# Kernel tuning notes

Hardware: AMD Instinct MI355X
Metric: run time of the kernel (lower is better)

Reference implementation:

```python
import jax, jax.numpy as jnp
import numpy as np

# irreps config (l<=1 only)
N, E = 20000, 400000
NS, NV = 64, 32          # node: 64x0e + 32x1o  (dim 64 + 96 = 160)
ES, EV = 8, 8            # edge: 8x0e + 8x1o    (dim 8 + 24 = 32)
HS, HV = 96, 32          # hidden: 96x0e + 32x1o (last HV scalars are gates)
GS = HS - HV             # post-gate scalar channels
INV_SQRT3 = float(1.0 / np.sqrt(3.0))  # w3j(1,1,0) normalization


def _tp_gate(xs, xv, ys, yv, Wss, Wvv, Wsv, Wvs):
    """FullyConnectedTensorProduct (paths 0x0->0, 1.1->0, 0x1->1, 1x0->1)
    with fan-in path normalization, followed by a gated nonlinearity:
    silu on scalars, sigmoid-gated vectors.
    xs:[*,u] xv:[*,u',3] ys:[*,v] yv:[*,v',3] -> (gs:[*,GS], gv:[*,HV,3])"""
    n_s = 1.0 / np.sqrt(Wss.shape[0] * Wss.shape[1] + Wvv.shape[0] * Wvv.shape[1])
    n_v = 1.0 / np.sqrt(Wsv.shape[0] * Wsv.shape[1] + Wvs.shape[0] * Wvs.shape[1])
    hs = (jnp.einsum('eu,ev,uvw->ew', xs, ys, Wss)
          + INV_SQRT3 * jnp.einsum('euk,evk,uvw->ew', xv, yv, Wvv)) * n_s
    hv = (jnp.einsum('eu,evk,uvw->ewk', xs, yv, Wsv)
          + jnp.einsum('euk,ev,uvw->ewk', xv, ys, Wvs)) * n_v
    gs = jax.nn.silu(hs[:, :GS])
    gates = jax.nn.sigmoid(hs[:, GS:])          # [*, HV]
    gv = hv * gates[:, :, None]
    return gs, gv


def _irrep_linear(s, v, Ws, Wv):
    """e3nn-style Linear: independent multiplicity mixing per irrep, 1/sqrt(fan_in)."""
    return (s @ Ws) / np.sqrt(Ws.shape[0]), jnp.einsum('nuk,uw->nwk', v, Wv) / np.sqrt(Wv.shape[0])


def setup_inputs() -> dict:
    key = jax.random.key(0)
    ks = jax.random.split(key, 16)
    inp = {
        'node_features': jax.random.normal(ks[0], (N, NS + 3 * NV), jnp.float32),
        'edge_attr_tensor': jax.random.normal(ks[1], (E, ES + 3 * EV), jnp.float32),
        'node_attr_scalar_raw': jax.random.normal(ks[2], (N, 1), jnp.float32),
        'edge_index': jax.random.randint(ks[3], (2, E), 0, N),
        # message TP weights: node (x) edge -> hidden
        'W_m_ss': jax.random.normal(ks[4], (NS, ES, HS), jnp.float32),
        'W_m_vv': jax.random.normal(ks[5], (NV, EV, HS), jnp.float32),
        'W_m_sv': jax.random.normal(ks[6], (NS, EV, HV), jnp.float32),
        'W_m_vs': jax.random.normal(ks[7], (NV, ES, HV), jnp.float32),
        # linear_messages_out: gate-out (GSx0e+HVx1o) -> hidden
        'Wl_ms': jax.random.normal(ks[8], (GS, HS), jnp.float32),
        'Wl_mv': jax.random.normal(ks[9], (HV, HV), jnp.float32),
        # update TP weights: node (x) hidden -> hidden
        'W_u_ss': jax.random.normal(ks[10], (NS, HS, HS), jnp.float32),
        'W_u_vv': jax.random.normal(ks[11], (NV, HV, HS), jnp.float32),
        'W_u_sv': jax.random.normal(ks[12], (NS, HV, HV), jnp.float32),
        'W_u_vs': jax.random.normal(ks[13], (NV, HS, HV), jnp.float32),
        # linear_update_out: gate-out -> node irreps
        'Wl_us': jax.random.normal(ks[14], (GS, NS), jnp.float32),
        'Wl_uv': jax.random.normal(ks[15], (HV, NV), jnp.float32),
    }
    return inp


def reference(node_features, edge_attr_tensor, node_attr_scalar_raw, edge_index,
              W_m_ss, W_m_vv, W_m_sv, W_m_vs, Wl_ms, Wl_mv,
              W_u_ss, W_u_vv, W_u_sv, W_u_vs, Wl_us, Wl_uv):
    n = node_features.shape[0]
    row, col = edge_index[0], edge_index[1]
    xs = node_features[:, :NS]                              # [N,NS]
    xv = node_features[:, NS:].reshape(n, NV, 3)            # [N,NV,3]
    es = edge_attr_tensor[:, :ES]                           # [E,ES]
    ev = edge_attr_tensor[:, ES:].reshape(-1, EV, 3)        # [E,EV,3]
    # gather source nodes, TP with edge attrs, gate
    ms, mv = _tp_gate(xs[col], xv[col], es, ev, W_m_ss, W_m_vv, W_m_sv, W_m_vs)
    ms, mv = _irrep_linear(ms, mv, Wl_ms, Wl_mv)            # -> hidden irreps
    # scatter-sum into destination nodes
    ags = jax.ops.segment_sum(ms, row, num_segments=n)      # [N,HS]
    agv = jax.ops.segment_sum(mv.reshape(-1, HV * 3), row, num_segments=n).reshape(n, HV, 3)
    # update TP: node (x) aggregated, gate, project back to node irreps
    us, uv = _tp_gate(xs, xv, ags, agv, W_u_ss, W_u_vv, W_u_sv, W_u_vs)
    us, uv = _irrep_linear(us, uv, Wl_us, Wl_uv)
    upd = jnp.concatenate([us, uv.reshape(n, NV * 3)], axis=-1)
    return node_features + upd
```

## Files before the change

kernel.cpp:

```cpp
#include <hip/hip_runtime.h>

#define NN 20000
#define NE 400000

typedef __attribute__((ext_vector_type(4))) float f32x4;
typedef _Float16 h2 __attribute__((ext_vector_type(2)));
typedef _Float16 h8 __attribute__((ext_vector_type(8)));

union H8 { h8 v; h2 p[4]; };

__device__ __forceinline__ float sigf(float x) { return 1.0f / (1.0f + __expf(-x)); }

__device__ __forceinline__ h8 rank1(_Float16 x, const h2 e[4]) {
    h2 xb = {x, x}; H8 f;
    #pragma unroll
    for (int j = 0; j < 4; ++j) f.p[j] = xb * e[j];
    return f.v;
}
__device__ __forceinline__ h8 rank3(_Float16 x0, _Float16 x1, _Float16 x2,
                                    const h2 e0[4], const h2 e1[4], const h2 e2[4]) {
    h2 x0b = {x0, x0}, x1b = {x1, x1}, x2b = {x2, x2}; H8 f;
    #pragma unroll
    for (int j = 0; j < 4; ++j) f.p[j] = x0b * e0[j] + x1b * e1[j] + x2b * e2[j];
    return f.v;
}
#define MFMA(a, b, c) __builtin_amdgcn_mfma_f32_16x16x32_f16(a, b, c, 0, 0, 0)

__global__ __launch_bounds__(256)
void prep_kernel(const float* __restrict__ s1, const float* __restrict__ s2,
                 int K1, int Kt, int Nw, float sc1, float sc2,
                 unsigned short* __restrict__ dst)
{
    __shared__ _Float16 tile[32][34];
    const int tx = threadIdx.x & 31, ty = threadIdx.x >> 5;
    const int K0 = blockIdx.x * 32, w0 = blockIdx.y * 32;
    #pragma unroll
    for (int r = 0; r < 4; ++r) {
        int K = K0 + ty + r * 8, w = w0 + tx;
        if (K < Kt && w < Nw) {
            float v = (K < K1) ? s1[(size_t)K * Nw + w] * sc1
                               : s2[(size_t)(K - K1) * Nw + w] * sc2;
            tile[ty + r * 8][tx] = (_Float16)v;
        }
    }
    __syncthreads();
    #pragma unroll
    for (int r = 0; r < 4; ++r) {
        int w = w0 + ty + r * 8, K = K0 + tx;
        if (w < Nw && K < Kt)
            dst[(size_t)w * Kt + K] = __builtin_bit_cast(unsigned short, tile[tx][ty + r * 8]);
    }
}

__global__ void hist_kernel(const int* __restrict__ eidx, int* __restrict__ counts)
{
    int e = blockIdx.x * 256 + threadIdx.x;
    if (e < NE) atomicAdd(&counts[eidx[e]], 1);
}

__global__ __launch_bounds__(1024)
void scan_kernel(int* __restrict__ data)
{
    __shared__ int wsum[16];
    __shared__ int s_carry;
    const int t = threadIdx.x, lane = t & 63, wv = t >> 6;
    if (t == 0) s_carry = 0;
    __syncthreads();
    for (int base = 0; base < NN; base += 1024) {
        int carry = s_carry;
        int idx = base + t;
        int v = (idx < NN) ? data[idx] : 0;
        int s = v;
        #pragma unroll
        for (int d = 1; d < 64; d <<= 1) {
            int x = __shfl_up(s, d, 64);
            if (lane >= d) s += x;
        }
        if (lane == 63) wsum[wv] = s;
        __syncthreads();
        if (t < 16) {
            int ws = wsum[t];
            #pragma unroll
            for (int d = 1; d < 16; d <<= 1) {
                int x = __shfl_up(ws, d, 64);
                if (t >= d) ws += x;
            }
            wsum[t] = ws;
        }
        __syncthreads();
        if (idx < NN) data[idx] = carry + (wv ? wsum[wv - 1] : 0) + s - v;
        if (t == 0) s_carry = carry + wsum[15];
        __syncthreads();
    }
}

__global__ void scatter_kernel(const int* __restrict__ eidx, int* __restrict__ cursor,
                               int* __restrict__ perm)
{
    int e = blockIdx.x * 256 + threadIdx.x;
    if (e < NE) {
        int r = eidx[e];
        int p = atomicAdd(&cursor[r], 1);
        perm[p] = e;
    }
}

template<int MB>
__device__ __forceinline__ void msg_gemmB(
    int ln, int okt,
    const _Float16 (*s_xsh)[68], const _Float16 (*s_xv01)[66], const _Float16 (*s_xv2)[34],
    const _Float16 (*s_esh)[8], const _Float16 (*s_evTh)[3][8],
    const unsigned short* __restrict__ wB, f32x4* acc)
{
    const unsigned short* b0p = wB + (size_t)ln * 768;
    const unsigned short* b1p = wB + (size_t)(16 + ln) * 768;

    h2 vv[6][4];
    #pragma unroll
    for (int m = 0; m < 6; ++m) {
        const int k = (MB + m) >> 2, e = (((MB + m) & 3) << 4) + ln;
        #pragma unroll
        for (int j = 0; j < 4; ++j) vv[m][j] = ((const h2*)s_evTh[e][k])[j];
    }
    #pragma unroll 4
    for (int ks = 0; ks < 16; ++ks) {
        const int ko = ks * 32 + okt * 8, u = ks * 4 + okt;
        h8 b0 = *(const h8*)(b0p + ko), b1 = *(const h8*)(b1p + ko);
        #pragma unroll
        for (int m = 0; m < 6; ++m) {
            const int e = (((MB + m) & 3) << 4) + ln;
            h8 a = rank1(s_xsh[e][u], vv[m]);
            acc[m * 2]     = MFMA(a, b0, acc[m * 2]);
            acc[m * 2 + 1] = MFMA(a, b1, acc[m * 2 + 1]);
        }
    }
    h2 ee[6][4];
    #pragma unroll
    for (int m = 0; m < 6; ++m) {
        const int e = (((MB + m) & 3) << 4) + ln;
        #pragma unroll
        for (int j = 0; j < 4; ++j) ee[m][j] = ((const h2*)s_esh[e])[j];
    }
    #pragma unroll 4
    for (int ks = 0; ks < 8; ++ks) {
        const int ko = 512 + ks * 32 + okt * 8, u = ks * 4 + okt;
        h8 b0 = *(const h8*)(b0p + ko), b1 = *(const h8*)(b1p + ko);
        #pragma unroll
        for (int m = 0; m < 6; ++m) {
            const int k = (MB + m) >> 2, e = (((MB + m) & 3) << 4) + ln;
            _Float16 x = (k < 2) ? s_xv01[e][u * 2 + k] : s_xv2[e][u];
            h8 a = rank1(x, ee[m]);
            acc[m * 2]     = MFMA(a, b0, acc[m * 2]);
            acc[m * 2 + 1] = MFMA(a, b1, acc[m * 2 + 1]);
        }
    }
}

__global__ __launch_bounds__(256, 3)
void msg_kernel(const float* __restrict__ nf, const float* __restrict__ ea,
                const int* __restrict__ eidx, const int* __restrict__ perm,
                const unsigned short* __restrict__ wA,
                const unsigned short* __restrict__ wB,
                float* __restrict__ agg)
{
    const int e0 = blockIdx.x * 64;
    const int t = threadIdx.x;
    const int wid = t >> 6, lane = t & 63, ln = lane & 15, okt = lane >> 4;

    __shared__ __align__(16) char smem[25600];
    _Float16 (*s_xsh)[68]    = (_Float16(*)[68])(smem);
    _Float16 (*s_xv01)[66]   = (_Float16(*)[66])(smem + 8704);
    _Float16 (*s_xv2)[34]    = (_Float16(*)[34])(smem + 17152);
    _Float16 (*s_esh)[8]     = (_Float16(*)[8])(smem + 21504);
    _Float16 (*s_evTh)[3][8] = (_Float16(*)[3][8])(smem + 22528);
    _Float16 (*s_msg)[162]   = (_Float16(*)[162])(smem);
    _Float16 (*s_gate)[33]   = (_Float16(*)[33])(smem + 20736);

    __shared__ int s_row[64], s_col[64], s_pe[64];

    if (t < 64) {
        int p = perm[e0 + t];
        s_pe[t] = p;
        s_row[t] = eidx[p];
        s_col[t] = eidx[NE + p];
    }
    __syncthreads();
    for (int i = t; i < 64 * 32; i += 256) {
        int e = i >> 5, c = i & 31;
        float v = ea[(size_t)s_pe[e] * 32 + c];
        if (c < 8) s_esh[e][c] = (_Float16)v;
        else { int d = c - 8; s_evTh[e][d % 3][d / 3] = (_Float16)v; }
    }
    for (int i = t; i < 64 * 40; i += 256) {
        int e = i / 40, q = i - e * 40;
        f32x4 f4 = *((const f32x4*)nf + (size_t)s_col[e] * 40 + q);
        if (q < 16) {
            #pragma unroll
            for (int j = 0; j < 4; ++j) s_xsh[e][q * 4 + j] = (_Float16)f4[j];
        } else {
            #pragma unroll
            for (int j = 0; j < 4; ++j) {
                int d = (q - 16) * 4 + j, u = d / 3, k = d - u * 3;
                if (k < 2) s_xv01[e][u * 2 + k] = (_Float16)f4[j];
                else       s_xv2[e][u] = (_Float16)f4[j];
            }
        }
    }
    __syncthreads();

    f32x4 acc[12] = {};

    if (wid < 2) {
        const unsigned short* wb = wA + (size_t)(wid * 48 + ln) * 768;
        h2 esv[4][4];
        #pragma unroll
        for (int m = 0; m < 4; ++m)
            #pragma unroll
            for (int j = 0; j < 4; ++j) esv[m][j] = ((const h2*)s_esh[m * 16 + ln])[j];
        #pragma unroll 4
        for (int ks = 0; ks < 16; ++ks) {
            const int ko = ks * 32 + okt * 8, u = ks * 4 + okt;
            h8 b0 = *(const h8*)(wb + ko);
            h8 b1 = *(const h8*)(wb + 16 * 768 + ko);
            h8 b2 = *(const h8*)(wb + 32 * 768 + ko);
            #pragma unroll
            for (int m = 0; m < 4; ++m) {
                h8 a = rank1(s_xsh[m * 16 + ln][u], esv[m]);
                acc[m * 3 + 0] = MFMA(a, b0, acc[m * 3 + 0]);
                acc[m * 3 + 1] = MFMA(a, b1, acc[m * 3 + 1]);
                acc[m * 3 + 2] = MFMA(a, b2, acc[m * 3 + 2]);
            }
        }
        h2 ev0[4][4], ev1[4][4], ev2[4][4];
        #pragma unroll
        for (int m = 0; m < 4; ++m)
            #pragma unroll
            for (int j = 0; j < 4; ++j) {
                ev0[m][j] = ((const h2*)s_evTh[m * 16 + ln][0])[j];
                ev1[m][j] = ((const h2*)s_evTh[m * 16 + ln][1])[j];
                ev2[m][j] = ((const h2*)s_evTh[m * 16 + ln][2])[j];
            }
        #pragma unroll 4
        for (int ks = 0; ks < 8; ++ks) {
            const int ko = 512 + ks * 32 + okt * 8, u = ks * 4 + okt;
            h8 b0 = *(const h8*)(wb + ko);
            h8 b1 = *(const h8*)(wb + 16 * 768 + ko);
            h8 b2 = *(const h8*)(wb + 32 * 768 + ko);
            #pragma unroll
            for (int m = 0; m < 4; ++m) {
                h2 x01 = *(const h2*)&s_xv01[m * 16 + ln][u * 2];
                h8 a = rank3(x01[0], x01[1], s_xv2[m * 16 + ln][u], ev0[m], ev1[m], ev2[m]);
                acc[m * 3 + 0] = MFMA(a, b0, acc[m * 3 + 0]);
                acc[m * 3 + 1] = MFMA(a, b1, acc[m * 3 + 1]);
                acc[m * 3 + 2] = MFMA(a, b2, acc[m * 3 + 2]);
            }
        }
    } else if (wid == 2) {
        msg_gemmB<0>(ln, okt, s_xsh, s_xv01, s_xv2, s_esh, s_evTh, wB, acc);
    } else {
        msg_gemmB<6>(ln, okt, s_xsh, s_xv01, s_xv2, s_esh, s_evTh, wB, acc);
    }

    __syncthreads();

    if (wid < 2) {
        #pragma unroll
        for (int m = 0; m < 4; ++m)
            #pragma unroll
            for (int j = 0; j < 3; ++j)
                #pragma unroll
                for (int r = 0; r < 4; ++r) {
                    int e = m * 16 + okt * 4 + r;
                    int w = wid * 48 + j * 16 + ln;
                    float h = acc[m * 3 + j][r];
                    if (w < 64) s_msg[e][w] = (_Float16)(h * sigf(h));
                    else        s_gate[e][w - 64] = (_Float16)sigf(h);
                }
    }
    __syncthreads();
    if (wid >= 2) {
        const int mb = (wid - 2) * 6;
        #pragma unroll
        for (int m = 0; m < 6; ++m) {
            int mm = mb + m, k = mm >> 2;
            #pragma unroll
            for (int tt = 0; tt < 2; ++tt)
                #pragma unroll
                for (int r = 0; r < 4; ++r) {
                    int e = ((mm & 3) << 4) + okt * 4 + r;
                    int w2 = tt * 16 + ln;
                    s_msg[e][64 + w2 * 3 + k] =
                        (_Float16)(acc[m * 2 + tt][r] * (float)s_gate[e][w2]);
                }
        }
    }
    __syncthreads();

    if (t < 160) {
        int cur = s_row[0];
        float a = (float)s_msg[0][t];
        for (int e = 1; e < 64; ++e) {
            int r = s_row[e];
            float v = (float)s_msg[e][t];
            if (r != cur) {
                atomicAdd(agg + (size_t)cur * 160 + t, a);
                cur = r; a = v;
            } else a += v;
        }
        atomicAdd(agg + (size_t)cur * 160 + t, a);
    }
}

template<int KH>
__global__ __launch_bounds__(256, 4)
void upd1_kernel(const float* __restrict__ nf, const float* __restrict__ agg,
                 const unsigned short* __restrict__ wA,
                 const unsigned short* __restrict__ wB,
                 const float* __restrict__ Wlms, const float* __restrict__ Wlmv,
                 float* __restrict__ hpart)
{
    const int n0 = blockIdx.x * 32;
    const int t = threadIdx.x;
    const int wid = t >> 6, lane = t & 63, ln = lane & 15, okt = lane >> 4;

    __shared__ __align__(16) _Float16 s_xsh[32][68];
    __shared__ __align__(16) _Float16 s_xv01[32][66];
    __shared__ __align__(16) _Float16 s_xv2[32][34];
    __shared__ __align__(16) _Float16 s_ash[32][104];
    __shared__ __align__(16) _Float16 s_avTh[32][3][40];

    for (int i = t; i < 32 * 40; i += 256) {
        int n = i / 40, q = i - n * 40;
        f32x4 f4 = *((const f32x4*)nf + (size_t)(n0 + n) * 40 + q);
        if (q < 16) {
            #pragma unroll
            for (int j = 0; j < 4; ++j) s_xsh[n][q * 4 + j] = (_Float16)f4[j];
        } else {
            #pragma unroll
            for (int j = 0; j < 4; ++j) {
                int d = (q - 16) * 4 + j, u = d / 3, k = d - u * 3;
                if (k < 2) s_xv01[n][u * 2 + k] = (_Float16)f4[j];
                else       s_xv2[n][u] = (_Float16)f4[j];
            }
        }
    }
    const float* agr = agg + (size_t)n0 * 160;
    #pragma unroll
    for (int r = 0; r < 12; ++r) {
        int o = t + r * 256;
        int n = o / 96, q = o - n * 96;
        float a = 0.f;
        #pragma unroll
        for (int u = 0; u < 64; ++u) a = fmaf(agr[n * 160 + u], Wlms[u * 96 + q], a);
        s_ash[n][q] = (_Float16)(a * 0.125f);
    }
    #pragma unroll
    for (int r = 0; r < 12; ++r) {
        int o = t + r * 256;
        int n = o / 96, q = o - n * 96, k = q >> 5, v = q & 31;
        float a = 0.f;
        #pragma unroll
        for (int u = 0; u < 32; ++u) a = fmaf(agr[n * 160 + 64 + u * 3 + k], Wlmv[u * 32 + v], a);
        s_avTh[n][k][v] = (_Float16)(a * 0.17677669529663687f);
    }
    __syncthreads();

    f32x4 acc[6] = {};
    constexpr int KB0 = KH ? 37 : 0;
    constexpr int KB1 = KH ? 64 : 37;

    if (wid < 2) {
        const unsigned short* wb = wA + (size_t)(wid * 48 + ln) * 7168;
        #pragma unroll 2
        for (int kb = KB0; kb < KB1; ++kb) {
            _Float16 x0 = s_xsh[ln][kb];
            _Float16 x1 = s_xsh[16 + ln][kb];
            #pragma unroll
            for (int p = 0; p < 3; ++p) {
                const int ko = kb * 96 + p * 32 + okt * 8;
                const int v0 = p * 32 + okt * 8;
                h8 b0 = *(const h8*)(wb + ko);
                h8 b1 = *(const h8*)(wb + 16 * 7168 + ko);
                h8 b2 = *(const h8*)(wb + 32 * 7168 + ko);
                h8 a0 = rank1(x0, (const h2*)&s_ash[ln][v0]);
                h8 a1 = rank1(x1, (const h2*)&s_ash[16 + ln][v0]);
                acc[0] = MFMA(a0, b0, acc[0]); acc[1] = MFMA(a0, b1, acc[1]); acc[2] = MFMA(a0, b2, acc[2]);
                acc[3] = MFMA(a1, b0, acc[3]); acc[4] = MFMA(a1, b1, acc[4]); acc[5] = MFMA(a1, b2, acc[5]);
            }
        }
        if (KH) {
            #pragma unroll 4
            for (int ks = 0; ks < 32; ++ks) {
                const int ko = 6144 + ks * 32 + okt * 8;
                const int v0 = okt * 8;
                h8 b0 = *(const h8*)(wb + ko);
                h8 b1 = *(const h8*)(wb + 16 * 7168 + ko);
                h8 b2 = *(const h8*)(wb + 32 * 7168 + ko);
                h2 xa = *(const h2*)&s_xv01[ln][ks * 2];
                h2 xb = *(const h2*)&s_xv01[16 + ln][ks * 2];
                h8 a0 = rank3(xa[0], xa[1], s_xv2[ln][ks],
                              (const h2*)&s_avTh[ln][0][v0], (const h2*)&s_avTh[ln][1][v0],
                              (const h2*)&s_avTh[ln][2][v0]);
                h8 a1 = rank3(xb[0], xb[1], s_xv2[16 + ln][ks],
                              (const h2*)&s_avTh[16 + ln][0][v0], (const h2*)&s_avTh[16 + ln][1][v0],
                              (const h2*)&s_avTh[16 + ln][2][v0]);
                acc[0] = MFMA(a0, b0, acc[0]); acc[1] = MFMA(a0, b1, acc[1]); acc[2] = MFMA(a0, b2, acc[2]);
                acc[3] = MFMA(a1, b0, acc[3]); acc[4] = MFMA(a1, b1, acc[4]); acc[5] = MFMA(a1, b2, acc[5]);
            }
        }
    } else {
        const unsigned short* bp = wB + (size_t)((wid - 2) * 16 + ln) * 5120;
        if (!KH) {
            #pragma unroll 2
            for (int ks = 0; ks < 64; ++ks) {
                const int ko = ks * 32 + okt * 8;
                const int v0 = okt * 8;
                h8 b = *(const h8*)(bp + ko);
                #pragma unroll
                for (int m = 0; m < 6; ++m) {
                    const int k = m >> 1, n = ((m & 1) << 4) + ln;
                    h8 a = rank1(s_xsh[n][ks], (const h2*)&s_avTh[n][k][v0]);
                    acc[m] = MFMA(a, b, acc[m]);
                }
            }
        } else {
            #pragma unroll 2
            for (int kb = 0; kb < 32; ++kb) {
                _Float16 xa[6];
                #pragma unroll
                for (int m = 0; m < 6; ++m) {
                    const int k = m >> 1, n = ((m & 1) << 4) + ln;
                    xa[m] = (k < 2) ? s_xv01[n][kb * 2 + k] : s_xv2[n][kb];
                }
                #pragma unroll
                for (int p = 0; p < 3; ++p) {
                    const int ko = 2048 + kb * 96 + p * 32 + okt * 8;
                    const int v0 = p * 32 + okt * 8;
                    h8 b = *(const h8*)(bp + ko);
                    #pragma unroll
                    for (int m = 0; m < 6; ++m) {
                        const int n = ((m & 1) << 4) + ln;
                        h8 a = rank1(xa[m], (const h2*)&s_ash[n][v0]);
                        acc[m] = MFMA(a, b, acc[m]);
                    }
                }
            }
        }
    }

    float* hp = hpart + ((size_t)KH * NN + n0) * 192;
    if (wid < 2) {
        #pragma unroll
        for (int m = 0; m < 2; ++m)
            #pragma unroll
            for (int j = 0; j < 3; ++j)
                #pragma unroll
                for (int r = 0; r < 4; ++r) {
                    int n = m * 16 + okt * 4 + r;
                    int w = wid * 48 + j * 16 + ln;
                    hp[(size_t)n * 192 + w] = acc[m * 3 + j][r];
                }
    } else {
        #pragma unroll
        for (int m = 0; m < 6; ++m)
            #pragma unroll
            for (int r = 0; r < 4; ++r) {
                int R = m * 16 + okt * 4 + r;
                int k = R >> 5, n = R & 31;
                int w2 = (wid - 2) * 16 + ln;
                hp[(size_t)n * 192 + 96 + w2 * 3 + k] = acc[m][r];
            }
    }
}

__global__ __launch_bounds__(256)
void upd2_kernel(const float* __restrict__ nf, const float* __restrict__ hpart,
                 const float* __restrict__ Wls, const float* __restrict__ Wlv,
                 float* __restrict__ out)
{
    const int n0 = blockIdx.x * 32;
    const int t = threadIdx.x;
    __shared__ float s_h[32][194];

    const float* h0 = hpart + (size_t)n0 * 192;
    const float* h1 = hpart + ((size_t)NN + n0) * 192;
    for (int i = t; i < 32 * 192; i += 256) {
        int n = i / 192, c = i - n * 192;
        s_h[n][c] = h0[(size_t)n * 192 + c] + h1[(size_t)n * 192 + c];
    }
    __syncthreads();
    for (int i = t; i < 32 * 96; i += 256) {
        int n = i / 96, w = i - n * 96;
        float h = s_h[n][w];
        s_h[n][w] = (w < 64) ? h * sigf(h) : sigf(h);
    }
    __syncthreads();
    for (int i = t; i < 32 * 96; i += 256) {
        int n = i / 96, wk = i - n * 96, w2 = wk / 3;
        s_h[n][96 + wk] *= s_h[n][64 + w2];
    }
    __syncthreads();
    for (int i = t; i < 32 * 64; i += 256) {
        int n = i >> 6, w = i & 63;
        float a = 0.f;
        #pragma unroll
        for (int u = 0; u < 64; ++u) a = fmaf(s_h[n][u], Wls[u * 64 + w], a);
        size_t o = (size_t)(n0 + n) * 160 + w;
        out[o] = nf[o] + a * 0.125f;
    }
    for (int i = t; i < 32 * 96; i += 256) {
        int n = i / 96, wk = i - n * 96, w = wk / 3, k = wk - w * 3;
        float a = 0.f;
        #pragma unroll
        for (int u = 0; u < 32; ++u) a = fmaf(s_h[n][96 + u * 3 + k], Wlv[u * 32 + w], a);
        size_t o = (size_t)(n0 + n) * 160 + 64 + wk;
        out[o] = nf[o] + a * 0.17677669529663687f;
    }
}

extern "C" void kernel_launch(void* const* d_in, const int* in_sizes, int n_in,
                              void* d_out, int out_size, void* d_ws, size_t ws_size,
                              hipStream_t stream) {
    const float* nf   = (const float*)d_in[0];
    const float* ea   = (const float*)d_in[1];
    const int*   eidx = (const int*)d_in[3];
    const float* Wmss = (const float*)d_in[4];
    const float* Wmvv = (const float*)d_in[5];
    const float* Wmsv = (const float*)d_in[6];
    const float* Wmvs = (const float*)d_in[7];
    const float* Wlms = (const float*)d_in[8];
    const float* Wlmv = (const float*)d_in[9];
    const float* Wuss = (const float*)d_in[10];
    const float* Wuvv = (const float*)d_in[11];
    const float* Wusv = (const float*)d_in[12];
    const float* Wuvs = (const float*)d_in[13];
    const float* Wlus = (const float*)d_in[14];
    const float* Wluv = (const float*)d_in[15];
    float* out = (float*)d_out;

    float* agg = (float*)d_ws;
    unsigned short* wAm = (unsigned short*)(agg + (size_t)NN * 160);
    unsigned short* wBm = wAm + 96 * 768;
    unsigned short* wAu = wBm + 32 * 768;
    unsigned short* wBu = wAu + (size_t)96 * 7168;
    int* counts = (int*)(wBu + (size_t)32 * 5120);
    int* perm   = counts + NN;
    float* hpart = (float*)(perm + NE);

    const float NSM = 0.03608439182435161f;
    const float NSU = 0.011811365506297619f;
    const float NVU = 0.013975424859373686f;
    const float S3  = 0.57735026918962576f;

    hipMemsetAsync(agg, 0, (size_t)NN * 160 * sizeof(float), stream);
    hipMemsetAsync(counts, 0, (size_t)NN * sizeof(int), stream);

    prep_kernel<<<dim3(24, 3), 256, 0, stream>>>(Wmss, Wmvv, 512, 768, 96, NSM, NSM * S3, wAm);
    prep_kernel<<<dim3(24, 1), 256, 0, stream>>>(Wmsv, Wmvs, 512, 768, 32, NSM, NSM, wBm);
    prep_kernel<<<dim3(224, 3), 256, 0, stream>>>(Wuss, Wuvv, 6144, 7168, 96, NSU, NSU * S3, wAu);
    prep_kernel<<<dim3(160, 1), 256, 0, stream>>>(Wusv, Wuvs, 2048, 5120, 32, NVU, NVU, wBu);

    hist_kernel<<<(NE + 255) / 256, 256, 0, stream>>>(eidx, counts);
    scan_kernel<<<1, 1024, 0, stream>>>(counts);
    scatter_kernel<<<(NE + 255) / 256, 256, 0, stream>>>(eidx, counts, perm);

    msg_kernel<<<NE / 64, 256, 0, stream>>>(nf, ea, eidx, perm, wAm, wBm, agg);

    upd1_kernel<0><<<NN / 32, 256, 0, stream>>>(nf, agg, wAu, wBu, Wlms, Wlmv, hpart);
    upd1_kernel<1><<<NN / 32, 256, 0, stream>>>(nf, agg, wAu, wBu, Wlms, Wlmv, hpart);
    upd2_kernel<<<NN / 32, 256, 0, stream>>>(nf, hpart, Wlus, Wluv, out);
}
```

Baseline: 653.7 us.

## Parallelize count scan, merge update halves into one launch, rebalance K split

Replaces the single-block serial prefix scan with a three-kernel block scan (per-block scan, serial scan of 20 block sums, add-back). Merges the two upd1 template launches into one 2D-grid launch selected by blockIdx.y and lowers the occupancy hint from 4 to 3 blocks. It also moves the first 5 kb iterations of the vector-path K loop from the KH=1 half to the KH=0 half to balance work between the halves. This cuts launch count and serialization but adds two small launches and may shift register allocation.

```diff
diff --git a/kernel.cpp b/kernel.cpp
--- a/kernel.cpp
+++ b/kernel.cpp
@@ -2,6 +2,7 @@
 
 #define NN 20000
 #define NE 400000
+#define NB_SCAN 20
 
 typedef __attribute__((ext_vector_type(4))) float f32x4;
 typedef _Float16 h2 __attribute__((ext_vector_type(2)));
@@ -59,39 +60,47 @@
 }
 
 __global__ __launch_bounds__(1024)
-void scan_kernel(int* __restrict__ data)
+void scan1_kernel(int* __restrict__ data, int* __restrict__ blksum)
 {
     __shared__ int wsum[16];
-    __shared__ int s_carry;
     const int t = threadIdx.x, lane = t & 63, wv = t >> 6;
-    if (t == 0) s_carry = 0;
-    __syncthreads();
-    for (int base = 0; base < NN; base += 1024) {
-        int carry = s_carry;
-        int idx = base + t;
-        int v = (idx < NN) ? data[idx] : 0;
-        int s = v;
-        #pragma unroll
-        for (int d = 1; d < 64; d <<= 1) {
-            int x = __shfl_up(s, d, 64);
-            if (lane >= d) s += x;
-        }
-        if (lane == 63) wsum[wv] = s;
-        __syncthreads();
-        if (t < 16) {
-            int ws = wsum[t];
-            #pragma unroll
-            for (int d = 1; d < 16; d <<= 1) {
-                int x = __shfl_up(ws, d, 64);
-                if (t >= d) ws += x;
-            }
-            wsum[t] = ws;
-        }
-        __syncthreads();
-        if (idx < NN) data[idx] = carry + (wv ? wsum[wv - 1] : 0) + s - v;
-        if (t == 0) s_carry = carry + wsum[15];
-        __syncthreads();
-    }
+    const int idx = blockIdx.x * 1024 + t;
+    int v = (idx < NN) ? data[idx] : 0;
+    int s = v;
+    #pragma unroll
+    for (int d = 1; d < 64; d <<= 1) {
+        int x = __shfl_up(s, d, 64);
+        if (lane >= d) s += x;
+    }
+    if (lane == 63) wsum[wv] = s;
+    __syncthreads();
+    if (t < 16) {
+        int ws = wsum[t];
+        #pragma unroll
+        for (int d = 1; d < 16; d <<= 1) {
+            int x = __shfl_up(ws, d, 64);
+            if (t >= d) ws += x;
+        }
+        wsum[t] = ws;
+    }
+    __syncthreads();
+    if (idx < NN) data[idx] = (wv ? wsum[wv - 1] : 0) + s - v;
+    if (t == 0) blksum[blockIdx.x] = wsum[15];
+}
+
+__global__ void scan2_kernel(int* __restrict__ blksum)
+{
+    if (threadIdx.x == 0) {
+        int run = 0;
+        for (int i = 0; i < NB_SCAN; ++i) { int x = blksum[i]; blksum[i] = run; run += x; }
+    }
+}
+
+__global__ __launch_bounds__(1024)
+void scan3_kernel(int* __restrict__ data, const int* __restrict__ blksum)
+{
+    int idx = blockIdx.x * 1024 + threadIdx.x;
+    if (idx < NN) data[idx] += blksum[blockIdx.x];
 }
 
 __global__ void scatter_kernel(const int* __restrict__ eidx, int* __restrict__ cursor,
@@ -312,22 +321,17 @@
 }
 
 template<int KH>
-__global__ __launch_bounds__(256, 4)
-void upd1_kernel(const float* __restrict__ nf, const float* __restrict__ agg,
-                 const unsigned short* __restrict__ wA,
-                 const unsigned short* __restrict__ wB,
-                 const float* __restrict__ Wlms, const float* __restrict__ Wlmv,
-                 float* __restrict__ hpart)
+__device__ __forceinline__ void upd1_body(
+    const float* __restrict__ nf, const float* __restrict__ agg,
+    const unsigned short* __restrict__ wA, const unsigned short* __restrict__ wB,
+    const float* __restrict__ Wlms, const float* __restrict__ Wlmv,
+    float* __restrict__ hpart,
+    _Float16 (*s_xsh)[68], _Float16 (*s_xv01)[66], _Float16 (*s_xv2)[34],
+    _Float16 (*s_ash)[104], _Float16 (*s_avTh)[3][40])
 {
     const int n0 = blockIdx.x * 32;
     const int t = threadIdx.x;
     const int wid = t >> 6, lane = t & 63, ln = lane & 15, okt = lane >> 4;
-
-    __shared__ __align__(16) _Float16 s_xsh[32][68];
-    __shared__ __align__(16) _Float16 s_xv01[32][66];
-    __shared__ __align__(16) _Float16 s_xv2[32][34];
-    __shared__ __align__(16) _Float16 s_ash[32][104];
-    __shared__ __align__(16) _Float16 s_avTh[32][3][40];
 
     for (int i = t; i < 32 * 40; i += 256) {
         int n = i / 40, q = i - n * 40;
@@ -423,26 +427,27 @@
                     acc[m] = MFMA(a, b, acc[m]);
                 }
             }
-        } else {
-            #pragma unroll 2
-            for (int kb = 0; kb < 32; ++kb) {
-                _Float16 xa[6];
+        }
+        constexpr int VB0 = KH ? 5 : 0;
+        constexpr int VB1 = KH ? 32 : 5;
+        #pragma unroll 2
+        for (int kb = VB0; kb < VB1; ++kb) {
+            _Float16 xa[6];
+            #pragma unroll
+            for (int m = 0; m < 6; ++m) {
+                const int k = m >> 1, n = ((m & 1) << 4) + ln;
+                xa[m] = (k < 2) ? s_xv01[n][kb * 2 + k] : s_xv2[n][kb];
+            }
+            #pragma unroll
+            for (int p = 0; p < 3; ++p) {
+                const int ko = 2048 + kb * 96 + p * 32 + okt * 8;
+                const int v0 = p * 32 + okt * 8;
+                h8 b = *(const h8*)(bp + ko);
                 #pragma unroll
                 for (int m = 0; m < 6; ++m) {
-                    const int k = m >> 1, n = ((m & 1) << 4) + ln;
-                    xa[m] = (k < 2) ? s_xv01[n][kb * 2 + k] : s_xv2[n][kb];
-                }
-                #pragma unroll
-                for (int p = 0; p < 3; ++p) {
-                    const int ko = 2048 + kb * 96 + p * 32 + okt * 8;
-                    const int v0 = p * 32 + okt * 8;
-                    h8 b = *(const h8*)(bp + ko);
-                    #pragma unroll
-                    for (int m = 0; m < 6; ++m) {
-                        const int n = ((m & 1) << 4) + ln;
-                        h8 a = rank1(xa[m], (const h2*)&s_ash[n][v0]);
-                        acc[m] = MFMA(a, b, acc[m]);
-                    }
+                    const int n = ((m & 1) << 4) + ln;
+                    h8 a = rank1(xa[m], (const h2*)&s_ash[n][v0]);
+                    acc[m] = MFMA(a, b, acc[m]);
                 }
             }
         }
@@ -471,6 +476,24 @@
                 hp[(size_t)n * 192 + 96 + w2 * 3 + k] = acc[m][r];
             }
     }
+}
+
+__global__ __launch_bounds__(256, 3)
+void upd1_kernel(const float* __restrict__ nf, const float* __restrict__ agg,
+                 const unsigned short* __restrict__ wA,
+                 const unsigned short* __restrict__ wB,
+                 const float* __restrict__ Wlms, const float* __restrict__ Wlmv,
+                 float* __restrict__ hpart)
+{
+    __shared__ __align__(16) _Float16 s_xsh[32][68];
+    __shared__ __align__(16) _Float16 s_xv01[32][66];
+    __shared__ __align__(16) _Float16 s_xv2[32][34];
+    __shared__ __align__(16) _Float16 s_ash[32][104];
+    __shared__ __align__(16) _Float16 s_avTh[32][3][40];
+    if (blockIdx.y == 0)
+        upd1_body<0>(nf, agg, wA, wB, Wlms, Wlmv, hpart, s_xsh, s_xv01, s_xv2, s_ash, s_avTh);
+    else
+        upd1_body<1>(nf, agg, wA, wB, Wlms, Wlmv, hpart, s_xsh, s_xv01, s_xv2, s_ash, s_avTh);
 }
 
 __global__ __launch_bounds__(256)
@@ -545,7 +568,8 @@
     unsigned short* wBu = wAu + (size_t)96 * 7168;
     int* counts = (int*)(wBu + (size_t)32 * 5120);
     int* perm   = counts + NN;
-    float* hpart = (float*)(perm + NE);
+    int* blksum = perm + NE;
+    float* hpart = (float*)(blksum + 64);
 
     const float NSM = 0.03608439182435161f;
     const float NSU = 0.011811365506297619f;
@@ -561,12 +585,13 @@
     prep_kernel<<<dim3(160, 1), 256, 0, stream>>>(Wusv, Wuvs, 2048, 5120, 32, NVU, NVU, wBu);
 
     hist_kernel<<<(NE + 255) / 256, 256, 0, stream>>>(eidx, counts);
-    scan_kernel<<<1, 1024, 0, stream>>>(counts);
+    scan1_kernel<<<NB_SCAN, 1024, 0, stream>>>(counts, blksum);
+    scan2_kernel<<<1, 64, 0, stream>>>(blksum);
+    scan3_kernel<<<NB_SCAN, 1024, 0, stream>>>(counts, blksum);
     scatter_kernel<<<(NE + 255) / 256, 256, 0, stream>>>(eidx, counts, perm);
 
     msg_kernel<<<NE / 64, 256, 0, stream>>>(nf, ea, eidx, perm, wAm, wBm, agg);
 
-    upd1_kernel<0><<<NN / 32, 256, 0, stream>>>(nf, agg, wAu, wBu, Wlms, Wlmv, hpart);
-    upd1_kernel<1><<<NN / 32, 256, 0, stream>>>(nf, agg, wAu, wBu, Wlms, Wlmv, hpart);
+    upd1_kernel<<<dim3(NN / 32, 2), 256, 0, stream>>>(nf, agg, wAu, wBu, Wlms, Wlmv, hpart);
     upd2_kernel<<<NN / 32, 256, 0, stream>>>(nf, hpart, Wlus, Wluv, out);
 }
```

New measurement: 692.6 us. 1.06x slower.
